# Kernel tuning notes

Measured on AMD Instinct MI355X. Metric: run time of the kernel, lower is better.

## Reference

```python
import jax, jax.numpy as jnp
import numpy as np

N_NODES = 100000
IN_DIM = 128
N_EDGES = 600000
HIDDEN = 128


def setup_inputs() -> dict:
    key = jax.random.key(0)
    k_z, k_e, k_w1, k_b1, k_w2, k_b2 = jax.random.split(key, 6)
    z = jax.random.normal(k_z, (N_NODES, IN_DIM), dtype=jnp.float32)
    edge_index = jax.random.randint(k_e, (2, N_EDGES), 0, N_NODES, dtype=jnp.int64)
    # torch.nn.Linear weights: W has shape (out, in), y = x @ W.T + b
    lim1 = 1.0 / np.sqrt(2 * IN_DIM)
    W1 = jax.random.uniform(k_w1, (HIDDEN, 2 * IN_DIM), jnp.float32, -lim1, lim1)
    b1 = jax.random.uniform(k_b1, (HIDDEN,), jnp.float32, -lim1, lim1)
    lim2 = 1.0 / np.sqrt(HIDDEN)
    W2 = jax.random.uniform(k_w2, (1, HIDDEN), jnp.float32, -lim2, lim2)
    b2 = jax.random.uniform(k_b2, (1,), jnp.float32, -lim2, lim2)
    return {"z": z, "edge_index": edge_index, "W1": W1, "b1": b1, "W2": W2, "b2": b2}


def reference(z, edge_index, W1, b1, W2, b2):
    src, dst = edge_index[0], edge_index[1]
    pair = jnp.concatenate([z[src], z[dst]], axis=1)        # [E, 2*in_dim]
    h = jax.nn.relu(pair @ W1.T + b1)                        # [E, 128]
    out = (h @ W2.T + b2).squeeze(-1)                        # [E]
    return out
```

## Files before the change

kernel.cpp:

```cpp
#include <hip/hip_runtime.h>

#define IN_DIM 128
#define NCOL   256

typedef __bf16 bfx8 __attribute__((ext_vector_type(8)));
typedef __bf16 bfx4 __attribute__((ext_vector_type(4)));
typedef float  f32x4 __attribute__((ext_vector_type(4)));

__global__ __launch_bounds__(256) void prep_w(
    const float* __restrict__ W1, __bf16* __restrict__ Weff)
{
    const int t   = threadIdx.x;
    const int n   = blockIdx.x * 32 + (t >> 3);
    const int k0  = (t & 7) * 16;
    const float* src = (n < 128) ? (W1 + n * 256 + k0) : (W1 + (n - 128) * 256 + 128 + k0);
    __bf16* dst = Weff + n * IN_DIM + k0;
#pragma unroll
    for (int k = 0; k < 16; k += 4) {
        float4 f = *(const float4*)(src + k);
        bfx4 b;
        b[0] = (__bf16)f.x; b[1] = (__bf16)f.y; b[2] = (__bf16)f.z; b[3] = (__bf16)f.w;
        *(bfx4*)(dst + k) = b;
    }
}

__global__ __launch_bounds__(256) void gemm_mfma(
    const float* __restrict__ z, const __bf16* __restrict__ Weff,
    const float* __restrict__ b1, __bf16* __restrict__ UV, int M)
{
    const int tid  = threadIdx.x;
    const int wave = tid >> 6;
    const int lane = tid & 63;
    const int l15  = lane & 15;
    const int q    = lane >> 4;
    const int n0   = wave * 64;
    const int m0   = blockIdx.x * 32;

    bfx8 wfrag[4][4];
#pragma unroll
    for (int nt = 0; nt < 4; ++nt) {
        const __bf16* wp = Weff + (n0 + nt * 16 + l15) * IN_DIM + q * 8;
#pragma unroll
        for (int kk = 0; kk < 4; ++kk)
            wfrag[nt][kk] = *(const bfx8*)(wp + kk * 32);
    }

    f32x4 bias[4];
#pragma unroll
    for (int nt = 0; nt < 4; ++nt) {
        const int nb = n0 + nt * 16 + q * 4;
        if (nb < 128) {
            float4 b = *(const float4*)(b1 + nb);
            bias[nt] = (f32x4){b.x, b.y, b.z, b.w};
        } else {
            bias[nt] = (f32x4){0.f, 0.f, 0.f, 0.f};
        }
    }

#pragma unroll
    for (int c = 0; c < 2; ++c) {
        const int m = m0 + c * 16 + l15;

        bfx8 zfrag[4];
#pragma unroll
        for (int kk = 0; kk < 4; ++kk) {
            const float* p = z + (size_t)m * IN_DIM + kk * 32 + q * 8;
            float4 f0 = *(const float4*)p;
            float4 f1 = *(const float4*)(p + 4);
            bfx8 a;
            a[0] = (__bf16)f0.x; a[1] = (__bf16)f0.y; a[2] = (__bf16)f0.z; a[3] = (__bf16)f0.w;
            a[4] = (__bf16)f1.x; a[5] = (__bf16)f1.y; a[6] = (__bf16)f1.z; a[7] = (__bf16)f1.w;
            zfrag[kk] = a;
        }

        f32x4 acc[4];
#pragma unroll
        for (int nt = 0; nt < 4; ++nt) acc[nt] = (f32x4){0.f, 0.f, 0.f, 0.f};

#pragma unroll
        for (int kk = 0; kk < 4; ++kk)
#pragma unroll
            for (int nt = 0; nt < 4; ++nt)
                acc[nt] = __builtin_amdgcn_mfma_f32_16x16x32_bf16(
                    wfrag[nt][kk], zfrag[kk], acc[nt], 0, 0, 0);

#pragma unroll
        for (int nt = 0; nt < 4; ++nt) {
            f32x4 t = acc[nt] + bias[nt];
            bfx4 o;
            o[0] = (__bf16)t[0]; o[1] = (__bf16)t[1];
            o[2] = (__bf16)t[2]; o[3] = (__bf16)t[3];
            *(bfx4*)(UV + (size_t)m * NCOL + n0 + nt * 16 + q * 4) = o;
        }
    }
}

__global__ __launch_bounds__(256) void edge_mlp(
    const __bf16* __restrict__ UV, const int* __restrict__ ei,
    const float* __restrict__ W2, const float* __restrict__ b2,
    float* __restrict__ out, int E)
{
    const int gt   = blockIdx.x * blockDim.x + threadIdx.x;
    const int lane = threadIdx.x & 15;
    const int g    = gt >> 4;
    const int e0   = g * 8;
    const int j0   = lane * 8;

    float ww[8];
    {
        float4 w0 = *(const float4*)(W2 + j0);
        float4 w1 = *(const float4*)(W2 + j0 + 4);
        ww[0] = w0.x; ww[1] = w0.y; ww[2] = w0.z; ww[3] = w0.w;
        ww[4] = w1.x; ww[5] = w1.y; ww[6] = w1.z; ww[7] = w1.w;
    }

    if (e0 >= E) return;

    const int4 sa = *(const int4*)(ei + e0);
    const int4 sb = *(const int4*)(ei + e0 + 4);
    const int4 da = *(const int4*)(ei + E + e0);
    const int4 db = *(const int4*)(ei + E + e0 + 4);
    const int sidx[8] = {sa.x, sa.y, sa.z, sa.w, sb.x, sb.y, sb.z, sb.w};
    const int didx[8] = {da.x, da.y, da.z, da.w, db.x, db.y, db.z, db.w};

    bfx8 u[8], v[8];
#pragma unroll
    for (int t = 0; t < 8; ++t) {
        u[t] = *(const bfx8*)(UV + (size_t)sidx[t] * NCOL + j0);
        v[t] = *(const bfx8*)(UV + (size_t)didx[t] * NCOL + 128 + j0);
    }

    float s[8];
#pragma unroll
    for (int t = 0; t < 8; ++t) {
        float acc = 0.f;
#pragma unroll
        for (int i = 0; i < 8; ++i)
            acc = fmaf(fmaxf((float)u[t][i] + (float)v[t][i], 0.f), ww[i], acc);
        s[t] = acc;
    }

#pragma unroll
    for (int d = 1; d < 16; d <<= 1)
#pragma unroll
        for (int t = 0; t < 8; ++t)
            s[t] += __shfl_xor(s[t], d);

    if (lane == 0) {
        const float bb = b2[0];
        float4 o0 = make_float4(s[0] + bb, s[1] + bb, s[2] + bb, s[3] + bb);
        float4 o1 = make_float4(s[4] + bb, s[5] + bb, s[6] + bb, s[7] + bb);
        *(float4*)(out + e0)     = o0;
        *(float4*)(out + e0 + 4) = o1;
    }
}

extern "C" void kernel_launch(void* const* d_in, const int* in_sizes, int n_in,
                              void* d_out, int out_size, void* d_ws, size_t ws_size,
                              hipStream_t stream)
{
    const float* z  = (const float*)d_in[0];
    const int*   ei = (const int*)d_in[1];
    const float* W1 = (const float*)d_in[2];
    const float* b1 = (const float*)d_in[3];
    const float* W2 = (const float*)d_in[4];
    const float* b2 = (const float*)d_in[5];
    float* out = (float*)d_out;

    const int M = in_sizes[0] / IN_DIM;
    const int E = in_sizes[1] / 2;

    __bf16* UV   = (__bf16*)d_ws;
    __bf16* Weff = UV + (size_t)M * NCOL;

    prep_w<<<8, 256, 0, stream>>>(W1, Weff);

    gemm_mfma<<<M / 32, 256, 0, stream>>>(z, Weff, b1, UV, M);

    const int groups  = (E + 7) / 8;
    const int eblocks = (groups * 16 + 255) / 256;
    edge_mlp<<<eblocks, 256, 0, stream>>>(UV, ei, W2, b2, out, E);
}
```

Before: 182.4 us.

## Stage GEMM output through LDS for coalesced stores and double-buffer z loads

The GEMM kernel now handles 64 rows per block as two 32-row chunks, swapping MFMA operand order so each lane owns a column. Results are written into a padded shared-memory tile and then stored to UV as coalesced 16-byte row segments. The second chunk's z loads are issued before the first chunk's epilogue so global latency overlaps with the store phase. This costs LDS traffic, two barriers per chunk and more registers, and halves the grid size. With M=100000 the last block has only 32 rows, which the has2 flag handles.

```diff
diff --git a/kernel.cpp b/kernel.cpp
--- a/kernel.cpp
+++ b/kernel.cpp
@@ -2,6 +2,7 @@
 
 #define IN_DIM 128
 #define NCOL   256
+#define TPITCH (NCOL + 8)
 
 typedef __bf16 bfx8 __attribute__((ext_vector_type(8)));
 typedef __bf16 bfx4 __attribute__((ext_vector_type(4)));
@@ -28,13 +29,15 @@
     const float* __restrict__ z, const __bf16* __restrict__ Weff,
     const float* __restrict__ b1, __bf16* __restrict__ UV, int M)
 {
+    __shared__ __bf16 tile[32][TPITCH];
+
     const int tid  = threadIdx.x;
     const int wave = tid >> 6;
     const int lane = tid & 63;
     const int l15  = lane & 15;
     const int q    = lane >> 4;
     const int n0   = wave * 64;
-    const int m0   = blockIdx.x * 32;
+    const int mbeg = blockIdx.x * 64;
 
     bfx8 wfrag[4][4];
 #pragma unroll
@@ -45,54 +48,89 @@
             wfrag[nt][kk] = *(const bfx8*)(wp + kk * 32);
     }
 
-    f32x4 bias[4];
+    float bias[4];
 #pragma unroll
     for (int nt = 0; nt < 4; ++nt) {
-        const int nb = n0 + nt * 16 + q * 4;
-        if (nb < 128) {
-            float4 b = *(const float4*)(b1 + nb);
-            bias[nt] = (f32x4){b.x, b.y, b.z, b.w};
-        } else {
-            bias[nt] = (f32x4){0.f, 0.f, 0.f, 0.f};
-        }
-    }
-
-#pragma unroll
-    for (int c = 0; c < 2; ++c) {
-        const int m = m0 + c * 16 + l15;
-
-        bfx8 zfrag[4];
-#pragma unroll
-        for (int kk = 0; kk < 4; ++kk) {
-            const float* p = z + (size_t)m * IN_DIM + kk * 32 + q * 8;
-            float4 f0 = *(const float4*)p;
-            float4 f1 = *(const float4*)(p + 4);
-            bfx8 a;
-            a[0] = (__bf16)f0.x; a[1] = (__bf16)f0.y; a[2] = (__bf16)f0.z; a[3] = (__bf16)f0.w;
-            a[4] = (__bf16)f1.x; a[5] = (__bf16)f1.y; a[6] = (__bf16)f1.z; a[7] = (__bf16)f1.w;
-            zfrag[kk] = a;
-        }
-
-        f32x4 acc[4];
-#pragma unroll
-        for (int nt = 0; nt < 4; ++nt) acc[nt] = (f32x4){0.f, 0.f, 0.f, 0.f};
-
-#pragma unroll
-        for (int kk = 0; kk < 4; ++kk)
-#pragma unroll
-            for (int nt = 0; nt < 4; ++nt)
-                acc[nt] = __builtin_amdgcn_mfma_f32_16x16x32_bf16(
-                    wfrag[nt][kk], zfrag[kk], acc[nt], 0, 0, 0);
-
-#pragma unroll
-        for (int nt = 0; nt < 4; ++nt) {
-            f32x4 t = acc[nt] + bias[nt];
-            bfx4 o;
-            o[0] = (__bf16)t[0]; o[1] = (__bf16)t[1];
-            o[2] = (__bf16)t[2]; o[3] = (__bf16)t[3];
-            *(bfx4*)(UV + (size_t)m * NCOL + n0 + nt * 16 + q * 4) = o;
-        }
-    }
+        const int n = n0 + nt * 16 + l15;
+        bias[nt] = (n < 128) ? b1[n] : 0.f;
+    }
+
+#define LOAD_A(afrag, mbase)                                                     \
+    {                                                                            \
+        _Pragma("unroll")                                                        \
+        for (int mt = 0; mt < 2; ++mt) {                                         \
+            _Pragma("unroll")                                                    \
+            for (int kk = 0; kk < 4; ++kk) {                                     \
+                const float* p = z + (size_t)((mbase) + mt * 16 + l15) * IN_DIM  \
+                                   + kk * 32 + q * 8;                            \
+                float4 f0 = *(const float4*)p;                                   \
+                float4 f1 = *(const float4*)(p + 4);                             \
+                bfx8 a;                                                          \
+                a[0] = (__bf16)f0.x; a[1] = (__bf16)f0.y;                        \
+                a[2] = (__bf16)f0.z; a[3] = (__bf16)f0.w;                        \
+                a[4] = (__bf16)f1.x; a[5] = (__bf16)f1.y;                        \
+                a[6] = (__bf16)f1.z; a[7] = (__bf16)f1.w;                        \
+                afrag[mt][kk] = a;                                               \
+            }                                                                    \
+        }                                                                        \
+    }
+
+#define MFMA_CHUNK(acc, afrag)                                                   \
+    {                                                                            \
+        _Pragma("unroll")                                                        \
+        for (int mt = 0; mt < 2; ++mt) {                                         \
+            _Pragma("unroll")                                                    \
+            for (int nt = 0; nt < 4; ++nt) acc[mt][nt] = (f32x4){0.f,0.f,0.f,0.f}; \
+        }                                                                        \
+        _Pragma("unroll")                                                        \
+        for (int kk = 0; kk < 4; ++kk)                                           \
+            _Pragma("unroll")                                                    \
+            for (int mt = 0; mt < 2; ++mt)                                       \
+                _Pragma("unroll")                                                \
+                for (int nt = 0; nt < 4; ++nt)                                   \
+                    acc[mt][nt] = __builtin_amdgcn_mfma_f32_16x16x32_bf16(       \
+                        afrag[mt][kk], wfrag[nt][kk], acc[mt][nt], 0, 0, 0);     \
+    }
+
+#define EPILOGUE(acc, mbase)                                                     \
+    {                                                                            \
+        _Pragma("unroll")                                                        \
+        for (int mt = 0; mt < 2; ++mt)                                           \
+            _Pragma("unroll")                                                    \
+            for (int nt = 0; nt < 4; ++nt) {                                     \
+                const int col = n0 + nt * 16 + l15;                              \
+                _Pragma("unroll")                                                \
+                for (int r = 0; r < 4; ++r)                                      \
+                    tile[mt * 16 + q * 4 + r][col] =                             \
+                        (__bf16)(acc[mt][nt][r] + bias[nt]);                     \
+            }                                                                    \
+        __syncthreads();                                                         \
+        _Pragma("unroll")                                                        \
+        for (int s = 0; s < 4; ++s) {                                            \
+            const int lin = s * 256 + tid;                                       \
+            const int row = lin >> 5;                                            \
+            const int c   = lin & 31;                                            \
+            bfx8 v = *(const bfx8*)&tile[row][c * 8];                            \
+            *(bfx8*)(UV + (size_t)((mbase) + row) * NCOL + c * 8) = v;           \
+        }                                                                        \
+        __syncthreads();                                                         \
+    }
+
+    bfx8  a0[2][4], a1[2][4];
+    f32x4 acc[2][4];
+    const bool has2 = (mbeg + 32 < M);
+
+    LOAD_A(a0, mbeg);
+    MFMA_CHUNK(acc, a0);
+    if (has2) LOAD_A(a1, mbeg + 32);
+    EPILOGUE(acc, mbeg);
+    if (has2) {
+        MFMA_CHUNK(acc, a1);
+        EPILOGUE(acc, mbeg + 32);
+    }
+#undef LOAD_A
+#undef MFMA_CHUNK
+#undef EPILOGUE
 }
 
 __global__ __launch_bounds__(256) void edge_mlp(
@@ -175,7 +213,8 @@
 
     prep_w<<<8, 256, 0, stream>>>(W1, Weff);
 
-    gemm_mfma<<<M / 32, 256, 0, stream>>>(z, Weff, b1, UV, M);
+    const int gblocks = (M + 63) / 64;
+    gemm_mfma<<<gblocks, 256, 0, stream>>>(z, Weff, b1, UV, M);
 
     const int groups  = (E + 7) / 8;
     const int eblocks = (groups * 16 + 255) / 256;
```

New measurement: 176.3 us. 3.3% less time.

## Split GEMM into single-wave blocks and stage output through LDS for coalesced stores

Applied to the files above, without the earlier changes.

The node GEMM now launches one 64-thread wave per block, each handling a 32-row by 64-column tile. The wave keeps both 16-row z fragments in registers and streams the W fragments per k-step, with the MFMA operands swapped so results come out column-major per lane. Results are written to a padded shared-memory tile and then stored as 16-byte row-contiguous chunks, replacing the scattered 8-byte stores. The cost is that each z row is read and converted by four separate blocks instead of being shared by the four waves of one block, which raises global z traffic.

```diff
diff --git a/kernel.cpp b/kernel.cpp
--- a/kernel.cpp
+++ b/kernel.cpp
@@ -2,6 +2,7 @@
 
 #define IN_DIM 128
 #define NCOL   256
+#define WPITCH 72
 
 typedef __bf16 bfx8 __attribute__((ext_vector_type(8)));
 typedef __bf16 bfx4 __attribute__((ext_vector_type(4)));
@@ -24,74 +25,79 @@
     }
 }
 
-__global__ __launch_bounds__(256) void gemm_mfma(
+__global__ __launch_bounds__(64) void gemm_mfma(
     const float* __restrict__ z, const __bf16* __restrict__ Weff,
     const float* __restrict__ b1, __bf16* __restrict__ UV, int M)
 {
-    const int tid  = threadIdx.x;
-    const int wave = tid >> 6;
-    const int lane = tid & 63;
+    __shared__ __bf16 tile[32][WPITCH];
+
+    const int lane = threadIdx.x;
     const int l15  = lane & 15;
     const int q    = lane >> 4;
-    const int n0   = wave * 64;
-    const int m0   = blockIdx.x * 32;
+    const int s    = blockIdx.x & 3;
+    const int m0   = (blockIdx.x >> 2) * 32;
+    const int n0   = s * 64;
 
-    bfx8 wfrag[4][4];
+    bfx8 zfrag[2][4];
 #pragma unroll
-    for (int nt = 0; nt < 4; ++nt) {
-        const __bf16* wp = Weff + (n0 + nt * 16 + l15) * IN_DIM + q * 8;
-#pragma unroll
-        for (int kk = 0; kk < 4; ++kk)
-            wfrag[nt][kk] = *(const bfx8*)(wp + kk * 32);
-    }
-
-    f32x4 bias[4];
-#pragma unroll
-    for (int nt = 0; nt < 4; ++nt) {
-        const int nb = n0 + nt * 16 + q * 4;
-        if (nb < 128) {
-            float4 b = *(const float4*)(b1 + nb);
-            bias[nt] = (f32x4){b.x, b.y, b.z, b.w};
-        } else {
-            bias[nt] = (f32x4){0.f, 0.f, 0.f, 0.f};
-        }
-    }
-
-#pragma unroll
-    for (int c = 0; c < 2; ++c) {
-        const int m = m0 + c * 16 + l15;
-
-        bfx8 zfrag[4];
+    for (int mt = 0; mt < 2; ++mt) {
 #pragma unroll
         for (int kk = 0; kk < 4; ++kk) {
-            const float* p = z + (size_t)m * IN_DIM + kk * 32 + q * 8;
+            const float* p = z + (size_t)(m0 + mt * 16 + l15) * IN_DIM + kk * 32 + q * 8;
             float4 f0 = *(const float4*)p;
             float4 f1 = *(const float4*)(p + 4);
             bfx8 a;
             a[0] = (__bf16)f0.x; a[1] = (__bf16)f0.y; a[2] = (__bf16)f0.z; a[3] = (__bf16)f0.w;
             a[4] = (__bf16)f1.x; a[5] = (__bf16)f1.y; a[6] = (__bf16)f1.z; a[7] = (__bf16)f1.w;
-            zfrag[kk] = a;
+            zfrag[mt][kk] = a;
+        }
+    }
+
+    float bias[4];
+#pragma unroll
+    for (int nt = 0; nt < 4; ++nt) {
+        const int n = n0 + nt * 16 + l15;
+        bias[nt] = (n < 128) ? b1[n] : 0.f;
+    }
+
+    f32x4 acc[2][4];
+#pragma unroll
+    for (int mt = 0; mt < 2; ++mt)
+#pragma unroll
+        for (int nt = 0; nt < 4; ++nt)
+            acc[mt][nt] = (f32x4){0.f, 0.f, 0.f, 0.f};
+
+#pragma unroll
+    for (int kk = 0; kk < 4; ++kk) {
+        bfx8 wfrag[4];
+#pragma unroll
+        for (int nt = 0; nt < 4; ++nt)
+            wfrag[nt] = *(const bfx8*)(Weff + (n0 + nt * 16 + l15) * IN_DIM
+                                       + kk * 32 + q * 8);
+#pragma unroll
+        for (int mt = 0; mt < 2; ++mt)
+#pragma unroll
+            for (int nt = 0; nt < 4; ++nt)
+                acc[mt][nt] = __builtin_amdgcn_mfma_f32_16x16x32_bf16(
+                    zfrag[mt][kk], wfrag[nt], acc[mt][nt], 0, 0, 0);
+    }
+
+#pragma unroll
+    for (int mt = 0; mt < 2; ++mt)
+#pragma unroll
+        for (int nt = 0; nt < 4; ++nt) {
+            const int col = nt * 16 + l15;
+#pragma unroll
+            for (int r = 0; r < 4; ++r)
+                tile[mt * 16 + q * 4 + r][col] = (__bf16)(acc[mt][nt][r] + bias[nt]);
         }
 
-        f32x4 acc[4];
 #pragma unroll
-        for (int nt = 0; nt < 4; ++nt) acc[nt] = (f32x4){0.f, 0.f, 0.f, 0.f};
-
-#pragma unroll
-        for (int kk = 0; kk < 4; ++kk)
-#pragma unroll
-            for (int nt = 0; nt < 4; ++nt)
-                acc[nt] = __builtin_amdgcn_mfma_f32_16x16x32_bf16(
-                    wfrag[nt][kk], zfrag[kk], acc[nt], 0, 0, 0);
-
-#pragma unroll
-        for (int nt = 0; nt < 4; ++nt) {
-            f32x4 t = acc[nt] + bias[nt];
-            bfx4 o;
-            o[0] = (__bf16)t[0]; o[1] = (__bf16)t[1];
-            o[2] = (__bf16)t[2]; o[3] = (__bf16)t[3];
-            *(bfx4*)(UV + (size_t)m * NCOL + n0 + nt * 16 + q * 4) = o;
-        }
+    for (int p = 0; p < 4; ++p) {
+        const int row = p * 8 + (lane >> 3);
+        const int c   = lane & 7;
+        bfx8 v = *(const bfx8*)&tile[row][c * 8];
+        *(bfx8*)(UV + (size_t)(m0 + row) * NCOL + n0 + c * 8) = v;
     }
 }
 
@@ -175,7 +181,8 @@
 
     prep_w<<<8, 256, 0, stream>>>(W1, Weff);
 
-    gemm_mfma<<<M / 32, 256, 0, stream>>>(z, Weff, b1, UV, M);
+    const int gblocks = (M / 32) * 4;
+    gemm_mfma<<<gblocks, 64, 0, stream>>>(z, Weff, b1, UV, M);
 
     const int groups  = (E + 7) / 8;
     const int eblocks = (groups * 16 + 255) / 256;
```

Result: faster. 177.5 us (-2.7%).
